# Kernel optimization log

Measured on AMD Instinct MI355X. Metric: run time of the kernel, lower is better.

The kernel has to match this reference:

```python
import jax, jax.numpy as jnp
import numpy as np

N_NODES = 50000
N_EDGES = 800000
D_FEAT = 64


def setup_inputs() -> dict:
    key = jax.random.key(0)
    k1, k2, k3, k4, k5 = jax.random.split(key, 5)
    features = jax.random.normal(k1, (N_NODES, D_FEAT), dtype=jnp.float32)
    src_idx = jax.random.randint(k2, (N_EDGES,), 0, N_NODES, dtype=jnp.int64)
    dst_idx = jax.random.randint(k3, (N_EDGES,), 0, N_NODES, dtype=jnp.int64)
    # MLP params: Linear(64,64) -> ReLU -> Linear(64,1) -> ReLU
    W1 = jax.random.normal(k4, (D_FEAT, D_FEAT), dtype=jnp.float32) * (1.0 / np.sqrt(D_FEAT))
    b1 = jnp.zeros((D_FEAT,), dtype=jnp.float32)
    W2 = jax.random.normal(k5, (D_FEAT, 1), dtype=jnp.float32) * (1.0 / np.sqrt(D_FEAT))
    b2 = jnp.zeros((1,), dtype=jnp.float32)
    return {"features": features, "src_idx": src_idx, "dst_idx": dst_idx,
            "W1": W1, "b1": b1, "W2": W2, "b2": b2}


def reference(features, src_idx, dst_idx, W1, b1, W2, b2):
    src_f = features[src_idx]            # [E, D]
    dst_f = features[dst_idx]            # [E, D]
    dif = src_f - dst_f                  # [E, D]
    h = jax.nn.relu(dif @ W1 + b1)       # [E, D]
    att = jax.nn.relu(h @ W2 + b2)       # [E, 1]
    att = jnp.exp(-att)                  # [E, 1]
    feature = att * dst_f                # [E, D]
    return feature
```

## Files before the change

kernel.cpp:

```cpp
#include <hip/hip_runtime.h>
#include <hip/hip_bf16.h>
#include <math.h>


#define D 64
#define NPB 64
#define U 4

typedef float nfloat4 __attribute__((ext_vector_type(4)));

__global__ __launch_bounds__(256) void node_proj_kernel(
    const float* __restrict__ F, const float* __restrict__ W1,
    float* __restrict__ P, int n_nodes)
{
    __shared__ float4 sW4[D * 16];
    __shared__ float4 sF4[NPB * 16];

    const int tid = threadIdx.x;
    const int base = blockIdx.x * NPB;
    const int nrows = min(NPB, n_nodes - base);

    const float4* W4 = (const float4*)W1;
#pragma unroll
    for (int i = 0; i < 4; ++i) sW4[tid + i * 256] = W4[tid + i * 256];

    const float4* Fg = (const float4*)(F + (long)base * D);
    const int totalf4 = nrows * 16;
    for (int i = tid; i < totalf4; i += 256) sF4[i] = Fg[i];
    __syncthreads();

    const int tx = tid & 15;
    const int ty = tid >> 4;

    float4 acc[4];
#pragma unroll
    for (int i = 0; i < 4; ++i) { acc[i].x = 0.f; acc[i].y = 0.f; acc[i].z = 0.f; acc[i].w = 0.f; }

#pragma unroll
    for (int k4 = 0; k4 < 16; ++k4) {
        float4 wr[4], fr[4];
#pragma unroll
        for (int r = 0; r < 4; ++r) wr[r] = sW4[(k4 * 4 + r) * 16 + tx];
#pragma unroll
        for (int i = 0; i < 4; ++i) fr[i] = sF4[(ty * 4 + i) * 16 + k4];
#pragma unroll
        for (int i = 0; i < 4; ++i) {
            acc[i].x += fr[i].x * wr[0].x + fr[i].y * wr[1].x + fr[i].z * wr[2].x + fr[i].w * wr[3].x;
            acc[i].y += fr[i].x * wr[0].y + fr[i].y * wr[1].y + fr[i].z * wr[2].y + fr[i].w * wr[3].y;
            acc[i].z += fr[i].x * wr[0].z + fr[i].y * wr[1].z + fr[i].z * wr[2].z + fr[i].w * wr[3].z;
            acc[i].w += fr[i].x * wr[0].w + fr[i].y * wr[1].w + fr[i].z * wr[2].w + fr[i].w * wr[3].w;
        }
    }

#pragma unroll
    for (int i = 0; i < 4; ++i) {
        const int n = ty * 4 + i;
        if (n < nrows) ((float4*)P)[(long)(base + n) * 16 + tx] = acc[i];
    }
}

__global__ __launch_bounds__(256, 4) void edge_kernel(
    const float4* __restrict__ P4, const float4* __restrict__ F4,
    const int* __restrict__ src_idx, const int* __restrict__ dst_idx,
    const float* __restrict__ b1, const float* __restrict__ W2,
    const float* __restrict__ b2v,
    float4* __restrict__ out4, int n_edges, int G)
{
    const int lane16 = threadIdx.x & 15;
    const int g = (blockIdx.x * blockDim.x + threadIdx.x) >> 4;

    const float4 b1f = ((const float4*)b1)[lane16];
    const float4 w2f = ((const float4*)W2)[lane16];
    const float b2s = b2v[0];

    int e[U]; bool ok[U]; long s[U], d[U];
#pragma unroll
    for (int j = 0; j < U; ++j) {
        e[j] = g + j * G;
        ok[j] = e[j] < n_edges;
        const int ee = ok[j] ? e[j] : 0;
        s[j] = (long)src_idx[ee];
        d[j] = (long)dst_idx[ee];
    }

    float4 ps[U], pd[U], fd[U];
#pragma unroll
    for (int j = 0; j < U; ++j) {
        ps[j] = P4[s[j] * 16 + lane16];
        pd[j] = P4[d[j] * 16 + lane16];
        fd[j] = F4[d[j] * 16 + lane16];
    }

#pragma unroll
    for (int j = 0; j < U; ++j) {
        const float hx = fmaxf(ps[j].x - pd[j].x + b1f.x, 0.f);
        const float hy = fmaxf(ps[j].y - pd[j].y + b1f.y, 0.f);
        const float hz = fmaxf(ps[j].z - pd[j].z + b1f.z, 0.f);
        const float hw = fmaxf(ps[j].w - pd[j].w + b1f.w, 0.f);

        float dot = hx * w2f.x + hy * w2f.y + hz * w2f.z + hw * w2f.w;
        dot += __shfl_xor(dot, 1);
        dot += __shfl_xor(dot, 2);
        dot += __shfl_xor(dot, 4);
        dot += __shfl_xor(dot, 8);

        const float a = __expf(-fmaxf(dot + b2s, 0.f));

        nfloat4 o;
        o.x = a * fd[j].x; o.y = a * fd[j].y; o.z = a * fd[j].z; o.w = a * fd[j].w;
        if (ok[j]) {
            nfloat4* dst = (nfloat4*)&out4[(long)e[j] * 16 + lane16];
            __builtin_nontemporal_store(o, dst);
        }
    }
}

extern "C" void kernel_launch(void* const* d_in, const int* in_sizes, int n_in,
                              void* d_out, int out_size, void* d_ws, size_t ws_size,
                              hipStream_t stream) {
    const float* features = (const float*)d_in[0];
    const int*   src_idx  = (const int*)d_in[1];
    const int*   dst_idx  = (const int*)d_in[2];
    const float* W1       = (const float*)d_in[3];
    const float* b1       = (const float*)d_in[4];
    const float* W2       = (const float*)d_in[5];
    const float* b2       = (const float*)d_in[6];
    float* out = (float*)d_out;

    const int n_nodes = in_sizes[0] / D;
    const int n_edges = in_sizes[1];

    float* P = (float*)d_ws;

    const int grid1 = (n_nodes + NPB - 1) / NPB;
    node_proj_kernel<<<grid1, 256, 0, stream>>>(features, W1, P, n_nodes);

    const int grid2 = (n_edges + 16 * U - 1) / (16 * U);
    const int G = grid2 * 16;
    edge_kernel<<<grid2, 256, 0, stream>>>((const float4*)P, (const float4*)features,
                                           src_idx, dst_idx, b1, W2, b2,
                                           (float4*)out, n_edges, G);
}
```

Before: 322.7 us.

## Store node projections and features as interleaved bf16 table for edge gathers

The node kernel now writes both the W1 projection and a copy of the raw features as bf16, interleaved per node in one 256-byte row of the workspace. The edge kernel gathers from this table instead of two fp32 arrays, which halves gather bytes and puts the dst projection and dst features on adjacent lines. The per-thread edge unroll of 4 is also removed in favour of one edge per 16-lane group with an early exit. The bf16 rounding of the features and the projection adds error to the output, and dropping the unroll reduces memory-level parallelism per thread.

```diff
diff --git a/kernel.cpp b/kernel.cpp
--- a/kernel.cpp
+++ b/kernel.cpp
@@ -5,13 +5,21 @@
 
 #define D 64
 #define NPB 64
-#define U 4
 
 typedef float nfloat4 __attribute__((ext_vector_type(4)));
 
+static __device__ __forceinline__ unsigned short f2bf(float f) {
+    unsigned u = __float_as_uint(f);
+    u += 0x7fffu + ((u >> 16) & 1u);
+    return (unsigned short)(u >> 16);
+}
+static __device__ __forceinline__ float bf2f(unsigned short b) {
+    return __uint_as_float(((unsigned)b) << 16);
+}
+
 __global__ __launch_bounds__(256) void node_proj_kernel(
     const float* __restrict__ F, const float* __restrict__ W1,
-    float* __restrict__ P, int n_nodes)
+    ushort4* __restrict__ T, int n_nodes)
 {
     __shared__ float4 sW4[D * 16];
     __shared__ float4 sF4[NPB * 16];
@@ -55,64 +63,68 @@
 #pragma unroll
     for (int i = 0; i < 4; ++i) {
         const int n = ty * 4 + i;
-        if (n < nrows) ((float4*)P)[(long)(base + n) * 16 + tx] = acc[i];
+        if (n < nrows) {
+            ushort4 pu;
+            pu.x = f2bf(acc[i].x); pu.y = f2bf(acc[i].y);
+            pu.z = f2bf(acc[i].z); pu.w = f2bf(acc[i].w);
+            T[(long)(base + n) * 32 + tx] = pu;
+        }
+    }
+
+#pragma unroll
+    for (int c = tid; c < NPB * 16; c += 256) {
+        const int n = c >> 4;
+        if (n < nrows) {
+            const int sub = c & 15;
+            const float4 f = sF4[c];
+            ushort4 fu;
+            fu.x = f2bf(f.x); fu.y = f2bf(f.y); fu.z = f2bf(f.z); fu.w = f2bf(f.w);
+            T[(long)(base + n) * 32 + 16 + sub] = fu;
+        }
     }
 }
 
-__global__ __launch_bounds__(256, 4) void edge_kernel(
-    const float4* __restrict__ P4, const float4* __restrict__ F4,
+__global__ __launch_bounds__(256) void edge_kernel(
+    const ushort4* __restrict__ T,
     const int* __restrict__ src_idx, const int* __restrict__ dst_idx,
     const float* __restrict__ b1, const float* __restrict__ W2,
     const float* __restrict__ b2v,
-    float4* __restrict__ out4, int n_edges, int G)
+    float4* __restrict__ out4, int n_edges)
 {
+    const int tid = blockIdx.x * blockDim.x + threadIdx.x;
     const int lane16 = threadIdx.x & 15;
-    const int g = (blockIdx.x * blockDim.x + threadIdx.x) >> 4;
+    const int e = tid >> 4;
+    if (e >= n_edges) return;
 
     const float4 b1f = ((const float4*)b1)[lane16];
     const float4 w2f = ((const float4*)W2)[lane16];
     const float b2s = b2v[0];
 
-    int e[U]; bool ok[U]; long s[U], d[U];
-#pragma unroll
-    for (int j = 0; j < U; ++j) {
-        e[j] = g + j * G;
-        ok[j] = e[j] < n_edges;
-        const int ee = ok[j] ? e[j] : 0;
-        s[j] = (long)src_idx[ee];
-        d[j] = (long)dst_idx[ee];
-    }
+    const long s = (long)src_idx[e];
+    const long d = (long)dst_idx[e];
 
-    float4 ps[U], pd[U], fd[U];
-#pragma unroll
-    for (int j = 0; j < U; ++j) {
-        ps[j] = P4[s[j] * 16 + lane16];
-        pd[j] = P4[d[j] * 16 + lane16];
-        fd[j] = F4[d[j] * 16 + lane16];
-    }
+    const ushort4 psu = T[s * 32 + lane16];
+    const ushort4 pdu = T[d * 32 + lane16];
+    const ushort4 fdu = T[d * 32 + 16 + lane16];
 
-#pragma unroll
-    for (int j = 0; j < U; ++j) {
-        const float hx = fmaxf(ps[j].x - pd[j].x + b1f.x, 0.f);
-        const float hy = fmaxf(ps[j].y - pd[j].y + b1f.y, 0.f);
-        const float hz = fmaxf(ps[j].z - pd[j].z + b1f.z, 0.f);
-        const float hw = fmaxf(ps[j].w - pd[j].w + b1f.w, 0.f);
+    const float hx = fmaxf(bf2f(psu.x) - bf2f(pdu.x) + b1f.x, 0.f);
+    const float hy = fmaxf(bf2f(psu.y) - bf2f(pdu.y) + b1f.y, 0.f);
+    const float hz = fmaxf(bf2f(psu.z) - bf2f(pdu.z) + b1f.z, 0.f);
+    const float hw = fmaxf(bf2f(psu.w) - bf2f(pdu.w) + b1f.w, 0.f);
 
-        float dot = hx * w2f.x + hy * w2f.y + hz * w2f.z + hw * w2f.w;
-        dot += __shfl_xor(dot, 1);
-        dot += __shfl_xor(dot, 2);
-        dot += __shfl_xor(dot, 4);
-        dot += __shfl_xor(dot, 8);
+    float dot = hx * w2f.x + hy * w2f.y + hz * w2f.z + hw * w2f.w;
+    dot += __shfl_xor(dot, 1);
+    dot += __shfl_xor(dot, 2);
+    dot += __shfl_xor(dot, 4);
+    dot += __shfl_xor(dot, 8);
 
-        const float a = __expf(-fmaxf(dot + b2s, 0.f));
+    const float a = __expf(-fmaxf(dot + b2s, 0.f));
 
-        nfloat4 o;
-        o.x = a * fd[j].x; o.y = a * fd[j].y; o.z = a * fd[j].z; o.w = a * fd[j].w;
-        if (ok[j]) {
-            nfloat4* dst = (nfloat4*)&out4[(long)e[j] * 16 + lane16];
-            __builtin_nontemporal_store(o, dst);
-        }
-    }
+    nfloat4 o;
+    o.x = a * bf2f(fdu.x); o.y = a * bf2f(fdu.y);
+    o.z = a * bf2f(fdu.z); o.w = a * bf2f(fdu.w);
+    nfloat4* dst = (nfloat4*)&out4[(long)e * 16 + lane16];
+    __builtin_nontemporal_store(o, dst);
 }
 
 extern "C" void kernel_launch(void* const* d_in, const int* in_sizes, int n_in,
@@ -130,14 +142,13 @@
     const int n_nodes = in_sizes[0] / D;
     const int n_edges = in_sizes[1];
 
-    float* P = (float*)d_ws;
+    ushort4* T = (ushort4*)d_ws;
 
     const int grid1 = (n_nodes + NPB - 1) / NPB;
-    node_proj_kernel<<<grid1, 256, 0, stream>>>(features, W1, P, n_nodes);
+    node_proj_kernel<<<grid1, 256, 0, stream>>>(features, W1, T, n_nodes);
 
-    const int grid2 = (n_edges + 16 * U - 1) / (16 * U);
-    const int G = grid2 * 16;
-    edge_kernel<<<grid2, 256, 0, stream>>>((const float4*)P, (const float4*)features,
-                                           src_idx, dst_idx, b1, W2, b2,
-                                           (float4*)out, n_edges, G);
+    const int groups_per_block = 256 / 16;
+    const int grid2 = (n_edges + groups_per_block - 1) / groups_per_block;
+    edge_kernel<<<grid2, 256, 0, stream>>>(T, src_idx, dst_idx,
+                                           b1, W2, b2, (float4*)out, n_edges);
 }
```

After: 298.9 us. -7.4%, faster.
